# Performance work log

Measured on AMD Instinct MI355X. Metric: run time of the kernel, lower is better.

Reference implementation:

```python
import jax, jax.numpy as jnp
import numpy as np

N = 100000
E = 1600000
ROUND = 2


def spmm(src, dst, x):
    # adj.matmul(x) with binary sparse adjacency given as edge list:
    # out[dst] += x[src]
    return jax.ops.segment_sum(x[src], dst, num_segments=N)


def setup_inputs() -> dict:
    key = jax.random.key(0)
    ks = jax.random.split(key, 8)
    x = jax.random.normal(ks[0], (N, 512), dtype=jnp.float32)
    W_embed = jax.random.normal(ks[1], (512, 64), dtype=jnp.float32) * (1.0 / np.sqrt(512))
    b_embed = jnp.zeros((64,), dtype=jnp.float32)
    W_cls = jax.random.normal(ks[2], (448, 40), dtype=jnp.float32) * (1.0 / np.sqrt(448))
    b_cls = jnp.zeros((40,), dtype=jnp.float32)
    adj_src = jax.random.randint(ks[3], (E,), 0, N, dtype=jnp.int32)
    adj_dst = jax.random.randint(ks[4], (E,), 0, N, dtype=jnp.int32)
    adj2_src = jax.random.randint(ks[5], (E,), 0, N, dtype=jnp.int32)
    adj2_dst = jax.random.randint(ks[6], (E,), 0, N, dtype=jnp.int32)
    return {"x": x, "W_embed": W_embed, "b_embed": b_embed, "W_cls": W_cls,
            "b_cls": b_cls, "adj_src": adj_src, "adj_dst": adj_dst,
            "adj2_src": adj2_src, "adj2_dst": adj2_dst}


def reference(x, W_embed, b_embed, W_cls, b_cls, adj_src, adj_dst, adj2_src, adj2_dst):
    # embed: Linear + ReLU
    h = jax.nn.relu(x @ W_embed + b_embed)  # [N, 64]
    hidden_reps = [h]
    for _ in range(ROUND):
        r1 = spmm(adj_src, adj_dst, h)      # 1-hop aggregation
        r2 = spmm(adj2_src, adj2_dst, h)    # 2-hop aggregation
        h = jnp.concatenate([r1, r2], axis=-1)
        hidden_reps.append(h)
    hf = jnp.concatenate(hidden_reps, axis=-1)  # [N, 64*(2^(ROUND+1)-1)] = [N, 448]
    # dropout is identity in eval mode
    logits = hf @ W_cls + b_cls
    return jax.nn.log_softmax(logits, axis=1)
```

## Files before the change

kernel.cpp:

```cpp
#include <hip/hip_runtime.h>
#include <hip/hip_bf16.h>

#define NN 100000
#define EE 1600000
#define NBK 196
#define BSH 9
#define EPB 4096
#define STG 10240
#define CAP 9216

using frag8 = __attribute__((ext_vector_type(8))) short;
using f32x4 = __attribute__((ext_vector_type(4))) float;

__device__ inline unsigned short f2bf(float f) {
    unsigned u = __float_as_uint(f);
    u = u + 0x7FFFu + ((u >> 16) & 1u);
    return (unsigned short)(u >> 16);
}
__device__ inline float bf2f(unsigned short u) {
    return __uint_as_float(((unsigned)u) << 16);
}
__device__ inline unsigned pack_bf16(float a, float b) {
    __hip_bfloat162 h = __float22bfloat162_rn(float2{a, b});
    union { __hip_bfloat162 h2; unsigned u; } c;
    c.h2 = h;
    return c.u;
}
__device__ inline unsigned char f2fp8(float v) {
    unsigned p = __builtin_amdgcn_cvt_pk_fp8_f32(v, v, 0, false);
    return (unsigned char)(p & 0xff);
}


__global__ __launch_bounds__(256) void binA_k(const int* __restrict__ s1,
                                              const int* __restrict__ d1,
                                              const int* __restrict__ s2,
                                              const int* __restrict__ d2,
                                              int* __restrict__ bcur,
                                              unsigned* __restrict__ tmp1,
                                              unsigned* __restrict__ tmp2) {
    __shared__ int lhist[NBK], lbase[NBK], gbase[NBK], lcur[NBK];
    __shared__ int sscan[256];
    __shared__ int stot;
    __shared__ uint2 stage[EPB];
    int adj = blockIdx.y;
    const int* ss = adj ? s2 : s1;
    const int* dd = adj ? d2 : d1;
    unsigned* tmp = adj ? tmp2 : tmp1;
    int t = threadIdx.x;
    for (int i = t; i < NBK; i += 256) { lhist[i] = 0; lcur[i] = 0; }
    __syncthreads();
    int e0 = blockIdx.x * EPB;
    int d[16], s[16];
    #pragma unroll
    for (int k = 0; k < 16; ++k) {
        int e = e0 + k * 256 + t;
        d[k] = (e < EE) ? dd[e] : -1;
        s[k] = (e < EE) ? ss[e] : 0;
        if (d[k] >= 0) atomicAdd(&lhist[d[k] >> BSH], 1);
    }
    __syncthreads();
    int hv = (t < NBK) ? lhist[t] : 0;
    sscan[t] = hv;
    __syncthreads();
    for (int off = 1; off < 256; off <<= 1) {
        int u = (t >= off) ? sscan[t - off] : 0;
        __syncthreads();
        sscan[t] += u;
        __syncthreads();
    }
    if (t < NBK) lbase[t] = sscan[t] - hv;
    if (t == NBK - 1) stot = sscan[t];
    __syncthreads();
    for (int i = t; i < NBK; i += 256)
        gbase[i] = lhist[i] ? atomicAdd(&bcur[adj * NBK + i], lhist[i]) : 0;
    __syncthreads();
    #pragma unroll
    for (int k = 0; k < 16; ++k) {
        if (d[k] >= 0) {
            int b = d[k] >> BSH;
            int pos = lbase[b] + atomicAdd(&lcur[b], 1);
            stage[pos] = make_uint2((unsigned)d[k], (unsigned)s[k]);
        }
    }
    __syncthreads();
    int tot = stot;
    for (int i = t; i < tot; i += 256) {
        uint2 u = stage[i];
        int b = u.x >> BSH;
        int off = gbase[b] + (i - lbase[b]);
        if (off < CAP)
            tmp[(size_t)b * CAP + off] = ((u.x & 511u) << 17) | u.y;
    }
}

__global__ __launch_bounds__(256) void binB_k(const unsigned* __restrict__ tmp1,
                                              const unsigned* __restrict__ tmp2,
                                              const int* __restrict__ bcur,
                                              int2* __restrict__ rse1,
                                              int2* __restrict__ rse2,
                                              int* __restrict__ csr1,
                                              int* __restrict__ csr2) {
    __shared__ int cnt[512], cur[512];
    __shared__ int sscan[256];
    __shared__ int stage[STG];
    int adj = blockIdx.y, b = blockIdx.x;
    const unsigned* tmp = adj ? tmp2 : tmp1;
    int2* rse = adj ? rse2 : rse1;
    int* csr  = adj ? csr2 : csr1;
    int t = threadIdx.x;
    int n0 = b << BSH;
    int n1 = n0 + 512; if (n1 > NN) n1 = NN;
    int nn = n1 - n0;
    int base = b * CAP;
    int count = bcur[adj * NBK + b];
    if (count > CAP) count = CAP;
    cnt[t] = 0; cnt[t + 256] = 0;
    __syncthreads();
    for (int i = t; i < count; i += 256)
        atomicAdd(&cnt[tmp[base + i] >> 17], 1);
    __syncthreads();
    int c0 = cnt[2 * t], c1 = cnt[2 * t + 1];
    int ps = c0 + c1;
    sscan[t] = ps;
    __syncthreads();
    for (int off = 1; off < 256; off <<= 1) {
        int u = (t >= off) ? sscan[t - off] : 0;
        __syncthreads();
        sscan[t] += u;
        __syncthreads();
    }
    int pe = sscan[t] - ps;
    int e0x = pe, e1x = pe + c0;
    if (2 * t < nn)     rse[n0 + 2 * t]     = make_int2(base + e0x, c0);
    if (2 * t + 1 < nn) rse[n0 + 2 * t + 1] = make_int2(base + e1x, c1);
    cur[2 * t] = e0x; cur[2 * t + 1] = e1x;
    __syncthreads();
    for (int i = t; i < count; i += 256) {
        unsigned u = tmp[base + i];
        int loc = atomicAdd(&cur[u >> 17], 1);
        int src = (int)(u & 0x1FFFFu);
        if (loc < STG) stage[loc] = src;
        else csr[base + loc] = src;
    }
    __syncthreads();
    int m = count < STG ? count : STG;
    for (int i = t; i < m; i += 256) csr[base + i] = stage[i];
}


__global__ void wprep_k(const float* __restrict__ W, unsigned short* __restrict__ Wbf,
                        const float* __restrict__ Wc, unsigned short* __restrict__ Wbig) {
    int blk = blockIdx.x;
    if (blk < 128) {
        int id = blk * 256 + threadIdx.x;
        if (id < 512 * 64) {
            int k = id >> 6, col = id & 63;
            int ch = k >> 3, el = k & 7;
            int cs = (ch & ~15) | ((ch & 15) ^ (col & 7));
            Wbf[col * 512 + cs * 8 + el] = f2bf(W[id]);
        }
    } else {
        int id = (blk - 128) * 256 + threadIdx.x;
        int k = id >> 7, col = id & 127;
        float v = 0.f;
        if (col < 40) v = Wc[k * 40 + col];
        else if (col < 80)  { if (k >= 64) v = Wc[(192 + k - 64) * 40 + (col - 40)]; }
        else if (col < 120) { if (k >= 64) v = Wc[(320 + k - 64) * 40 + (col - 80)]; }
        int ch = k >> 3, el = k & 7;
        int phys = (ch & ~7) | ((ch & 7) ^ (col & 7));
        Wbig[col * 192 + phys * 8 + el] = f2bf(v);
    }
}


__global__ __launch_bounds__(256) void embed_k(const float* __restrict__ x,
                                               const unsigned short* __restrict__ Wbf,
                                               const float* __restrict__ bias,
                                               unsigned short* __restrict__ hcat,
                                               unsigned char* __restrict__ h0f8) {
    __shared__ unsigned short sW[64 * 128];
    int tid = threadIdx.x;
    int lane = tid & 63, wave = tid >> 6;
    int row0 = blockIdx.x * 64;
    f32x4 acc[4];
    #pragma unroll
    for (int n = 0; n < 4; n++) acc[n] = (f32x4){0.f, 0.f, 0.f, 0.f};

    int arow = row0 + wave * 16 + (lane & 15);
    bool valid = arow < NN;
    const float* xrow = x + (size_t)(valid ? arow : 0) * 512 + (lane >> 4) * 8;

    for (int kt = 0; kt < 4; ++kt) {
        for (int q = tid; q < 1024; q += 256) {
            int col = q >> 4, c = q & 15;
            ((uint4*)sW)[q] = ((const uint4*)Wbf)[col * 64 + kt * 16 + c];
        }
        __syncthreads();
        #pragma unroll
        for (int kk = 0; kk < 4; ++kk) {
            const float4* px = (const float4*)(xrow + kt * 128 + kk * 32);
            float4 p0 = px[0], p1 = px[1];
            frag8 a;
            unsigned* au = (unsigned*)&a;
            if (valid) {
                au[0] = pack_bf16(p0.x, p0.y);
                au[1] = pack_bf16(p0.z, p0.w);
                au[2] = pack_bf16(p1.x, p1.y);
                au[3] = pack_bf16(p1.z, p1.w);
            } else {
                au[0] = 0; au[1] = 0; au[2] = 0; au[3] = 0;
            }
            #pragma unroll
            for (int n = 0; n < 4; n++) {
                int col = n * 16 + (lane & 15);
                int bc = (kk * 4 + (lane >> 4)) ^ (col & 7);
                frag8 b = *(const frag8*)&sW[(col * 16 + bc) * 8];
                acc[n] = __builtin_amdgcn_mfma_f32_16x16x32_bf16(a, b, acc[n], 0, 0, 0);
            }
        }
        __syncthreads();
    }
    #pragma unroll
    for (int n = 0; n < 4; n++) {
        int col = n * 16 + (lane & 15);
        float bv = bias[col];
        #pragma unroll
        for (int i = 0; i < 4; i++) {
            int r = row0 + wave * 16 + (lane >> 4) * 4 + i;
            if (r < NN) {
                float vv = acc[n][i] + bv;
                vv = vv > 0.f ? vv : 0.f;
                hcat[(size_t)r * 192 + col] = f2bf(vv);
                h0f8[(size_t)r * 64 + col] = f2fp8(vv);
            }
        }
    }
}


__device__ inline void gacc8f8(float* a, uint2 u) {
    a[0] += __builtin_amdgcn_cvt_f32_fp8(u.x, 0);
    a[1] += __builtin_amdgcn_cvt_f32_fp8(u.x, 1);
    a[2] += __builtin_amdgcn_cvt_f32_fp8(u.x, 2);
    a[3] += __builtin_amdgcn_cvt_f32_fp8(u.x, 3);
    a[4] += __builtin_amdgcn_cvt_f32_fp8(u.y, 0);
    a[5] += __builtin_amdgcn_cvt_f32_fp8(u.y, 1);
    a[6] += __builtin_amdgcn_cvt_f32_fp8(u.y, 2);
    a[7] += __builtin_amdgcn_cvt_f32_fp8(u.y, 3);
}


__global__ __launch_bounds__(256) void round1_k(const unsigned char* __restrict__ h8,
                                                unsigned short* __restrict__ hc,
                                                const int2* __restrict__ rse1,
                                                const int* __restrict__ csr1,
                                                const int2* __restrict__ rse2,
                                                const int* __restrict__ csr2) {
    int wave = threadIdx.x >> 6, lane = threadIdx.x & 63;
    int row = blockIdx.x * 4 + wave;
    int g = lane >> 3, gl = lane & 7;

    int2 v1r = rse1[row], v2r = rse2[row];
    int s1 = v1r.x, c1 = v1r.y, e1 = s1 + c1;
    int s2 = v2r.x, c2 = v2r.y, e2 = s2 + c2;
    int idx1 = 0, idx2 = 0;
    if (lane < c1) idx1 = csr1[s1 + lane];
    if (lane < c2) idx2 = csr2[s2 + lane];
    int cnt1 = c1 < 64 ? c1 : 64, cnt2 = c2 < 64 ? c2 : 64;

    float a1[8] = {0.f, 0.f, 0.f, 0.f, 0.f, 0.f, 0.f, 0.f};
    float a2[8] = {0.f, 0.f, 0.f, 0.f, 0.f, 0.f, 0.f, 0.f};

    {
        int j0 = g, j1 = 8 + g;
        int x10 = __shfl(idx1, j0), x11 = __shfl(idx1, j1);
        int x20 = __shfl(idx2, j0), x21 = __shfl(idx2, j1);
        uint2 u10 = *((const uint2*)(h8 + (size_t)x10 * 64) + gl);
        uint2 u11 = *((const uint2*)(h8 + (size_t)x11 * 64) + gl);
        uint2 u20 = *((const uint2*)(h8 + (size_t)x20 * 64) + gl);
        uint2 u21 = *((const uint2*)(h8 + (size_t)x21 * 64) + gl);
        if (j0 < cnt1) gacc8f8(a1, u10);
        if (j1 < cnt1) gacc8f8(a1, u11);
        if (j0 < cnt2) gacc8f8(a2, u20);
        if (j1 < cnt2) gacc8f8(a2, u21);
    }
    int nq1 = (cnt1 + 7) >> 3, nq2 = (cnt2 + 7) >> 3;
    int nq = nq1 > nq2 ? nq1 : nq2;
    for (int q = 2; q < nq; ++q) {
        int j = q * 8 + g;
        int y1 = __shfl(idx1, j), y2 = __shfl(idx2, j);
        uint2 w1 = *((const uint2*)(h8 + (size_t)y1 * 64) + gl);
        uint2 w2 = *((const uint2*)(h8 + (size_t)y2 * 64) + gl);
        if (j < cnt1) gacc8f8(a1, w1);
        if (j < cnt2) gacc8f8(a2, w2);
    }
    for (int t0 = s1 + 64; t0 < e1; t0 += 64) {
        int rem = e1 - t0;
        int idxv = 0;
        if (lane < rem) idxv = csr1[t0 + lane];
        int cnt = rem < 64 ? rem : 64;
        int nqt = (cnt + 7) >> 3;
        for (int q = 0; q < nqt; ++q) {
            int j = q * 8 + g;
            int s0 = __shfl(idxv, j);
            uint2 u = *((const uint2*)(h8 + (size_t)s0 * 64) + gl);
            if (j < cnt) gacc8f8(a1, u);
        }
    }
    for (int t0 = s2 + 64; t0 < e2; t0 += 64) {
        int rem = e2 - t0;
        int idxv = 0;
        if (lane < rem) idxv = csr2[t0 + lane];
        int cnt = rem < 64 ? rem : 64;
        int nqt = (cnt + 7) >> 3;
        for (int q = 0; q < nqt; ++q) {
            int j = q * 8 + g;
            int s0 = __shfl(idxv, j);
            uint2 u = *((const uint2*)(h8 + (size_t)s0 * 64) + gl);
            if (j < cnt) gacc8f8(a2, u);
        }
    }

    #pragma unroll
    for (int i = 0; i < 8; ++i) {
        a1[i] += __shfl_xor(a1[i], 8);
        a1[i] += __shfl_xor(a1[i], 16);
        a1[i] += __shfl_xor(a1[i], 32);
        a2[i] += __shfl_xor(a2[i], 8);
        a2[i] += __shfl_xor(a2[i], 16);
        a2[i] += __shfl_xor(a2[i], 32);
    }
    if (lane < 8) {
        uint4 o;
        o.x = pack_bf16(a1[0], a1[1]);
        o.y = pack_bf16(a1[2], a1[3]);
        o.z = pack_bf16(a1[4], a1[5]);
        o.w = pack_bf16(a1[6], a1[7]);
        *(uint4*)(hc + (size_t)row * 192 + 64 + lane * 8) = o;
    } else if (lane < 16) {
        int l = lane - 8;
        uint4 o;
        o.x = pack_bf16(a2[0], a2[1]);
        o.y = pack_bf16(a2[2], a2[3]);
        o.z = pack_bf16(a2[4], a2[5]);
        o.w = pack_bf16(a2[6], a2[7]);
        *(uint4*)(hc + (size_t)row * 192 + 128 + l * 8) = o;
    }
}


__global__ __launch_bounds__(256) void gemm_k(const unsigned short* __restrict__ hcat,
                                              const unsigned short* __restrict__ Wbig,
                                              const float* __restrict__ bc,
                                              float* __restrict__ logits,
                                              unsigned char* __restrict__ zf8) {
    __shared__ unsigned short sA[64 * 64];
    __shared__ unsigned short sB[128 * 64];
    int tid = threadIdx.x;
    int lane = tid & 63, wave = tid >> 6;
    int row0 = blockIdx.x * 64;
    f32x4 acc[8];
    #pragma unroll
    for (int n = 0; n < 8; n++) acc[n] = (f32x4){0.f, 0.f, 0.f, 0.f};

    for (int kt = 0; kt < 3; ++kt) {
        #pragma unroll
        for (int q = tid; q < 512; q += 256) {
            int r = q >> 3, c = q & 7;
            int phys = c ^ (r & 7);
            ((uint4*)sA)[r * 8 + phys] = ((const uint4*)hcat)[(size_t)(row0 + r) * 24 + kt * 8 + c];
        }
        #pragma unroll
        for (int q = tid; q < 1024; q += 256) {
            int col = q >> 3, c = q & 7;
            ((uint4*)sB)[q] = ((const uint4*)Wbig)[col * 24 + kt * 8 + c];
        }
        __syncthreads();
        #pragma unroll
        for (int kk = 0; kk < 2; ++kk) {
            int ar = wave * 16 + (lane & 15);
            int ac = (kk * 4 + (lane >> 4)) ^ (ar & 7);
            frag8 a = *(const frag8*)&sA[(ar * 8 + ac) * 8];
            #pragma unroll
            for (int n = 0; n < 8; n++) {
                int col = n * 16 + (lane & 15);
                int bcc = (kk * 4 + (lane >> 4)) ^ (col & 7);
                frag8 b = *(const frag8*)&sB[(col * 8 + bcc) * 8];
                acc[n] = __builtin_amdgcn_mfma_f32_16x16x32_bf16(a, b, acc[n], 0, 0, 0);
            }
        }
        __syncthreads();
    }
    #pragma unroll
    for (int n = 0; n < 8; n++) {
        int col = n * 16 + (lane & 15);
        float bv = (col < 40) ? bc[col] : 0.f;
        #pragma unroll
        for (int i = 0; i < 4; i++) {
            int r = row0 + wave * 16 + (lane >> 4) * 4 + i;
            if (r < NN) {
                float vv = acc[n][i];
                if (col < 40) {
                    logits[(size_t)r * 40 + col] = vv + bv;
                } else if (col < 80) {
                    zf8[(size_t)r * 128 + (col - 40)] = f2fp8(vv);
                } else if (col < 120) {
                    zf8[(size_t)r * 128 + 64 + (col - 80)] = f2fp8(vv);
                }
            }
        }
    }
}


__global__ __launch_bounds__(256) void round2_k(const unsigned char* __restrict__ z8,
                                                const int2* __restrict__ rse1,
                                                const int* __restrict__ csr1,
                                                const int2* __restrict__ rse2,
                                                const int* __restrict__ csr2,
                                                float* __restrict__ logits) {
    int wave = threadIdx.x >> 6, lane = threadIdx.x & 63;
    int row = blockIdx.x * 4 + wave;
    int g = lane >> 3, gl = lane & 7;

    int2 v1r = rse1[row], v2r = rse2[row];
    int s1 = v1r.x, c1 = v1r.y, e1 = s1 + c1;
    int s2 = v2r.x, c2 = v2r.y, e2 = s2 + c2;
    int idx1 = 0, idx2 = 0;
    if (lane < c1) idx1 = csr1[s1 + lane];
    if (lane < c2) idx2 = csr2[s2 + lane];
    int cnt1 = c1 < 64 ? c1 : 64, cnt2 = c2 < 64 ? c2 : 64;

    float a[8] = {0.f, 0.f, 0.f, 0.f, 0.f, 0.f, 0.f, 0.f};

    {
        int j0 = g, j1 = 8 + g;
        int x10 = __shfl(idx1, j0), x11 = __shfl(idx1, j1);
        int x20 = __shfl(idx2, j0), x21 = __shfl(idx2, j1);
        uint2 u10 = *((const uint2*)(z8 + (size_t)x10 * 128) + gl);
        uint2 u11 = *((const uint2*)(z8 + (size_t)x11 * 128) + gl);
        uint2 u20 = *((const uint2*)(z8 + (size_t)x20 * 128 + 64) + gl);
        uint2 u21 = *((const uint2*)(z8 + (size_t)x21 * 128 + 64) + gl);
        if (j0 < cnt1) gacc8f8(a, u10);
        if (j1 < cnt1) gacc8f8(a, u11);
        if (j0 < cnt2) gacc8f8(a, u20);
        if (j1 < cnt2) gacc8f8(a, u21);
    }
    int nq1 = (cnt1 + 7) >> 3, nq2 = (cnt2 + 7) >> 3;
    int nq = nq1 > nq2 ? nq1 : nq2;
    for (int q = 2; q < nq; ++q) {
        int j = q * 8 + g;
        int y1 = __shfl(idx1, j), y2 = __shfl(idx2, j);
        uint2 w1 = *((const uint2*)(z8 + (size_t)y1 * 128) + gl);
        uint2 w2 = *((const uint2*)(z8 + (size_t)y2 * 128 + 64) + gl);
        if (j < cnt1) gacc8f8(a, w1);
        if (j < cnt2) gacc8f8(a, w2);
    }
    for (int t0 = s1 + 64; t0 < e1; t0 += 64) {
        int rem = e1 - t0;
        int idxv = 0;
        if (lane < rem) idxv = csr1[t0 + lane];
        int cnt = rem < 64 ? rem : 64;
        int nqt = (cnt + 7) >> 3;
        for (int q = 0; q < nqt; ++q) {
            int j = q * 8 + g;
            int s0 = __shfl(idxv, j);
            uint2 u = *((const uint2*)(z8 + (size_t)s0 * 128) + gl);
            if (j < cnt) gacc8f8(a, u);
        }
    }
    for (int t0 = s2 + 64; t0 < e2; t0 += 64) {
        int rem = e2 - t0;
        int idxv = 0;
        if (lane < rem) idxv = csr2[t0 + lane];
        int cnt = rem < 64 ? rem : 64;
        int nqt = (cnt + 7) >> 3;
        for (int q = 0; q < nqt; ++q) {
            int j = q * 8 + g;
            int s0 = __shfl(idxv, j);
            uint2 u = *((const uint2*)(z8 + (size_t)s0 * 128 + 64) + gl);
            if (j < cnt) gacc8f8(a, u);
        }
    }

    #pragma unroll
    for (int i = 0; i < 8; ++i) {
        a[i] += __shfl_xor(a[i], 8);
        a[i] += __shfl_xor(a[i], 16);
        a[i] += __shfl_xor(a[i], 32);
    }

    bool act = lane < 5;
    float v[8];
    if (act) {
        float4 b0 = *(const float4*)(logits + (size_t)row * 40 + lane * 8);
        float4 b1 = *(const float4*)(logits + (size_t)row * 40 + lane * 8 + 4);
        v[0] = b0.x + a[0]; v[1] = b0.y + a[1]; v[2] = b0.z + a[2]; v[3] = b0.w + a[3];
        v[4] = b1.x + a[4]; v[5] = b1.y + a[5]; v[6] = b1.z + a[6]; v[7] = b1.w + a[7];
    } else {
        #pragma unroll
        for (int i = 0; i < 8; ++i) v[i] = -1e30f;
    }
    float m = fmaxf(fmaxf(fmaxf(v[0], v[1]), fmaxf(v[2], v[3])),
                    fmaxf(fmaxf(v[4], v[5]), fmaxf(v[6], v[7])));
    m = fmaxf(m, __shfl_xor(m, 1));
    m = fmaxf(m, __shfl_xor(m, 2));
    m = fmaxf(m, __shfl_xor(m, 4));
    float es = 0.f;
    if (act) {
        #pragma unroll
        for (int i = 0; i < 8; ++i) es += __expf(v[i] - m);
    }
    es += __shfl_xor(es, 1);
    es += __shfl_xor(es, 2);
    es += __shfl_xor(es, 4);
    float ls = __logf(es);
    if (act) {
        float4 o0, o1;
        o0.x = v[0] - m - ls; o0.y = v[1] - m - ls; o0.z = v[2] - m - ls; o0.w = v[3] - m - ls;
        o1.x = v[4] - m - ls; o1.y = v[5] - m - ls; o1.z = v[6] - m - ls; o1.w = v[7] - m - ls;
        *(float4*)(logits + (size_t)row * 40 + lane * 8)     = o0;
        *(float4*)(logits + (size_t)row * 40 + lane * 8 + 4) = o1;
    }
}


extern "C" void kernel_launch(void* const* d_in, const int* in_sizes, int n_in,
                              void* d_out, int out_size, void* d_ws, size_t ws_size,
                              hipStream_t stream) {
    const float* x       = (const float*)d_in[0];
    const float* W_embed = (const float*)d_in[1];
    const float* b_embed = (const float*)d_in[2];
    const float* W_cls   = (const float*)d_in[3];
    const float* b_cls   = (const float*)d_in[4];
    const int* a1src = (const int*)d_in[5];
    const int* a1dst = (const int*)d_in[6];
    const int* a2src = (const int*)d_in[7];
    const int* a2dst = (const int*)d_in[8];

    float* logits = (float*)d_out;
    float* ws = (float*)d_ws;

    const size_t OFF_HCAT = 0;
    const size_t OFF_H0F8 = 9600000;
    const size_t OFF_ZF8  = 11200000;
    const size_t OFF_RSE1 = 14400000;
    const size_t OFF_RSE2 = 14600000;
    const size_t OFF_BC   = 14800000;
    const size_t OFF_CSR1 = 14800392;
    const size_t OFF_CSR2 = 16606728;
    const size_t OFF_TMP1 = 18413064;
    const size_t OFF_TMP2 = 20219400;
    const size_t OFF_WBF  = 22025736;
    const size_t OFF_WBIG = 22042120;

    unsigned short* hcat = (unsigned short*)(ws + OFF_HCAT);
    unsigned char*  h0f8 = (unsigned char*)(ws + OFF_H0F8);
    unsigned char*  zf8  = (unsigned char*)(ws + OFF_ZF8);
    int2* rse1 = (int2*)(ws + OFF_RSE1);
    int2* rse2 = (int2*)(ws + OFF_RSE2);
    int*  bcur = (int*)(ws + OFF_BC);
    int*  csr1 = (int*)(ws + OFF_CSR1);
    int*  csr2 = (int*)(ws + OFF_CSR2);
    unsigned* tmp1 = (unsigned*)(ws + OFF_TMP1);
    unsigned* tmp2 = (unsigned*)(ws + OFF_TMP2);
    unsigned short* wbf  = (unsigned short*)(ws + OFF_WBF);
    unsigned short* wbig = (unsigned short*)(ws + OFF_WBIG);

    hipMemsetAsync(ws + OFF_BC, 0, 392 * 4, stream);

    const int NBA = (EE + EPB - 1) / EPB;

    binA_k<<<dim3(NBA, 2), 256, 0, stream>>>(a1src, a1dst, a2src, a2dst, bcur, tmp1, tmp2);
    binB_k<<<dim3(NBK, 2), 256, 0, stream>>>(tmp1, tmp2, bcur, rse1, rse2, csr1, csr2);

    wprep_k<<<224, 256, 0, stream>>>(W_embed, wbf, W_cls, wbig);
    embed_k<<<(NN + 63) / 64, 256, 0, stream>>>(x, wbf, b_embed, hcat, h0f8);

    round1_k<<<NN / 4, 256, 0, stream>>>(h0f8, hcat, rse1, csr1, rse2, csr2);
    gemm_k<<<(NN + 63) / 64, 256, 0, stream>>>(hcat, wbig, b_cls, logits, zf8);
    round2_k<<<NN / 4, 256, 0, stream>>>(zf8, rse1, csr1, rse2, csr2, logits);
}
```

Baseline: 252.9 us.

## Merge prep kernels horizontally and widen gather loads to 16-byte per lane

Merges the edge-binning and weight-prep kernels into one launch, and the CSR build and embedding GEMM into a second launch, so independent work shares a grid and two launches go away. The CSR build drops its shared-memory staging and writes straight to global memory. The gather kernels now have each lane load 16 fp8 bytes instead of 8, so 16 neighbours are processed per wave step instead of 8. The wider loads mean fewer load instructions and fewer loop iterations, but one more shuffle-reduction stage and more registers per lane.

Result: slower. 379.9 us (+50.2%).

```diff
diff --git a/kernel.cpp b/kernel.cpp
--- a/kernel.cpp
+++ b/kernel.cpp
@@ -6,7 +6,7 @@
 #define NBK 196
 #define BSH 9
 #define EPB 4096
-#define STG 10240
+#define NBA 391
 #define CAP 9216
 
 using frag8 = __attribute__((ext_vector_type(8))) short;
@@ -16,9 +16,6 @@
     unsigned u = __float_as_uint(f);
     u = u + 0x7FFFu + ((u >> 16) & 1u);
     return (unsigned short)(u >> 16);
-}
-__device__ inline float bf2f(unsigned short u) {
-    return __uint_as_float(((unsigned)u) << 16);
 }
 __device__ inline unsigned pack_bf16(float a, float b) {
     __hip_bfloat162 h = __float22bfloat162_rn(float2{a, b});
@@ -32,25 +29,56 @@
 }
 
 
-__global__ __launch_bounds__(256) void binA_k(const int* __restrict__ s1,
-                                              const int* __restrict__ d1,
-                                              const int* __restrict__ s2,
-                                              const int* __restrict__ d2,
-                                              int* __restrict__ bcur,
-                                              unsigned* __restrict__ tmp1,
-                                              unsigned* __restrict__ tmp2) {
+__global__ __launch_bounds__(256) void prep1_k(const int* __restrict__ s1,
+                                               const int* __restrict__ d1,
+                                               const int* __restrict__ s2,
+                                               const int* __restrict__ d2,
+                                               int* __restrict__ bcur,
+                                               unsigned* __restrict__ tmp1,
+                                               unsigned* __restrict__ tmp2,
+                                               const float* __restrict__ W,
+                                               unsigned short* __restrict__ Wbf,
+                                               const float* __restrict__ Wc,
+                                               unsigned short* __restrict__ Wbig) {
     __shared__ int lhist[NBK], lbase[NBK], gbase[NBK], lcur[NBK];
     __shared__ int sscan[256];
     __shared__ int stot;
     __shared__ uint2 stage[EPB];
-    int adj = blockIdx.y;
+    int blk = blockIdx.x;
+    int t = threadIdx.x;
+
+    if (blk >= 2 * NBA) {
+        int wb = blk - 2 * NBA;
+        if (wb < 128) {
+            int id = wb * 256 + t;
+            if (id < 512 * 64) {
+                int k = id >> 6, col = id & 63;
+                int ch = k >> 3, el = k & 7;
+                int cs = (ch & ~15) | ((ch & 15) ^ (col & 7));
+                Wbf[col * 512 + cs * 8 + el] = f2bf(W[id]);
+            }
+        } else {
+            int id = (wb - 128) * 256 + t;
+            int k = id >> 7, col = id & 127;
+            float v = 0.f;
+            if (col < 40) v = Wc[k * 40 + col];
+            else if (col < 80)  { if (k >= 64) v = Wc[(192 + k - 64) * 40 + (col - 40)]; }
+            else if (col < 120) { if (k >= 64) v = Wc[(320 + k - 64) * 40 + (col - 80)]; }
+            int ch = k >> 3, el = k & 7;
+            int phys = (ch & ~7) | ((ch & 7) ^ (col & 7));
+            Wbig[col * 192 + phys * 8 + el] = f2bf(v);
+        }
+        return;
+    }
+
+    int adj = blk / NBA;
+    int chunk = blk % NBA;
     const int* ss = adj ? s2 : s1;
     const int* dd = adj ? d2 : d1;
     unsigned* tmp = adj ? tmp2 : tmp1;
-    int t = threadIdx.x;
     for (int i = t; i < NBK; i += 256) { lhist[i] = 0; lcur[i] = 0; }
     __syncthreads();
-    int e0 = blockIdx.x * EPB;
+    int e0 = chunk * EPB;
     int d[16], s[16];
     #pragma unroll
     for (int k = 0; k < 16; ++k) {
@@ -94,95 +122,67 @@
     }
 }
 
-__global__ __launch_bounds__(256) void binB_k(const unsigned* __restrict__ tmp1,
-                                              const unsigned* __restrict__ tmp2,
-                                              const int* __restrict__ bcur,
-                                              int2* __restrict__ rse1,
-                                              int2* __restrict__ rse2,
-                                              int* __restrict__ csr1,
-                                              int* __restrict__ csr2) {
-    __shared__ int cnt[512], cur[512];
-    __shared__ int sscan[256];
-    __shared__ int stage[STG];
-    int adj = blockIdx.y, b = blockIdx.x;
-    const unsigned* tmp = adj ? tmp2 : tmp1;
-    int2* rse = adj ? rse2 : rse1;
-    int* csr  = adj ? csr2 : csr1;
-    int t = threadIdx.x;
-    int n0 = b << BSH;
-    int n1 = n0 + 512; if (n1 > NN) n1 = NN;
-    int nn = n1 - n0;
-    int base = b * CAP;
-    int count = bcur[adj * NBK + b];
-    if (count > CAP) count = CAP;
-    cnt[t] = 0; cnt[t + 256] = 0;
-    __syncthreads();
-    for (int i = t; i < count; i += 256)
-        atomicAdd(&cnt[tmp[base + i] >> 17], 1);
-    __syncthreads();
-    int c0 = cnt[2 * t], c1 = cnt[2 * t + 1];
-    int ps = c0 + c1;
-    sscan[t] = ps;
-    __syncthreads();
-    for (int off = 1; off < 256; off <<= 1) {
-        int u = (t >= off) ? sscan[t - off] : 0;
-        __syncthreads();
-        sscan[t] += u;
-        __syncthreads();
-    }
-    int pe = sscan[t] - ps;
-    int e0x = pe, e1x = pe + c0;
-    if (2 * t < nn)     rse[n0 + 2 * t]     = make_int2(base + e0x, c0);
-    if (2 * t + 1 < nn) rse[n0 + 2 * t + 1] = make_int2(base + e1x, c1);
-    cur[2 * t] = e0x; cur[2 * t + 1] = e1x;
-    __syncthreads();
-    for (int i = t; i < count; i += 256) {
-        unsigned u = tmp[base + i];
-        int loc = atomicAdd(&cur[u >> 17], 1);
-        int src = (int)(u & 0x1FFFFu);
-        if (loc < STG) stage[loc] = src;
-        else csr[base + loc] = src;
-    }
-    __syncthreads();
-    int m = count < STG ? count : STG;
-    for (int i = t; i < m; i += 256) csr[base + i] = stage[i];
-}
-
-
-__global__ void wprep_k(const float* __restrict__ W, unsigned short* __restrict__ Wbf,
-                        const float* __restrict__ Wc, unsigned short* __restrict__ Wbig) {
-    int blk = blockIdx.x;
-    if (blk < 128) {
-        int id = blk * 256 + threadIdx.x;
-        if (id < 512 * 64) {
-            int k = id >> 6, col = id & 63;
-            int ch = k >> 3, el = k & 7;
-            int cs = (ch & ~15) | ((ch & 15) ^ (col & 7));
-            Wbf[col * 512 + cs * 8 + el] = f2bf(W[id]);
-        }
-    } else {
-        int id = (blk - 128) * 256 + threadIdx.x;
-        int k = id >> 7, col = id & 127;
-        float v = 0.f;
-        if (col < 40) v = Wc[k * 40 + col];
-        else if (col < 80)  { if (k >= 64) v = Wc[(192 + k - 64) * 40 + (col - 40)]; }
-        else if (col < 120) { if (k >= 64) v = Wc[(320 + k - 64) * 40 + (col - 80)]; }
-        int ch = k >> 3, el = k & 7;
-        int phys = (ch & ~7) | ((ch & 7) ^ (col & 7));
-        Wbig[col * 192 + phys * 8 + el] = f2bf(v);
-    }
-}
-
-
-__global__ __launch_bounds__(256) void embed_k(const float* __restrict__ x,
+
+__global__ __launch_bounds__(256) void prep2_k(const unsigned* __restrict__ tmp1,
+                                               const unsigned* __restrict__ tmp2,
+                                               const int* __restrict__ bcur,
+                                               int2* __restrict__ rse1,
+                                               int2* __restrict__ rse2,
+                                               int* __restrict__ csr1,
+                                               int* __restrict__ csr2,
+                                               const float* __restrict__ x,
                                                const unsigned short* __restrict__ Wbf,
                                                const float* __restrict__ bias,
                                                unsigned short* __restrict__ hcat,
                                                unsigned char* __restrict__ h0f8) {
+    __shared__ int cnt[512], cur[512];
+    __shared__ int sscan[256];
     __shared__ unsigned short sW[64 * 128];
-    int tid = threadIdx.x;
-    int lane = tid & 63, wave = tid >> 6;
-    int row0 = blockIdx.x * 64;
+    int blk = blockIdx.x;
+    int t = threadIdx.x;
+
+    if (blk < 2 * NBK) {
+        int adj = blk / NBK, b = blk % NBK;
+        const unsigned* tmp = adj ? tmp2 : tmp1;
+        int2* rse = adj ? rse2 : rse1;
+        int* csr  = adj ? csr2 : csr1;
+        int n0 = b << BSH;
+        int n1 = n0 + 512; if (n1 > NN) n1 = NN;
+        int nn = n1 - n0;
+        int base = b * CAP;
+        int count = bcur[adj * NBK + b];
+        if (count > CAP) count = CAP;
+        cnt[t] = 0; cnt[t + 256] = 0;
+        __syncthreads();
+        for (int i = t; i < count; i += 256)
+            atomicAdd(&cnt[tmp[base + i] >> 17], 1);
+        __syncthreads();
+        int c0 = cnt[2 * t], c1 = cnt[2 * t + 1];
+        int ps = c0 + c1;
+        sscan[t] = ps;
+        __syncthreads();
+        for (int off = 1; off < 256; off <<= 1) {
+            int u = (t >= off) ? sscan[t - off] : 0;
+            __syncthreads();
+            sscan[t] += u;
+            __syncthreads();
+        }
+        int pe = sscan[t] - ps;
+        int e0x = pe, e1x = pe + c0;
+        if (2 * t < nn)     rse[n0 + 2 * t]     = make_int2(base + e0x, c0);
+        if (2 * t + 1 < nn) rse[n0 + 2 * t + 1] = make_int2(base + e1x, c1);
+        cur[2 * t] = e0x; cur[2 * t + 1] = e1x;
+        __syncthreads();
+        for (int i = t; i < count; i += 256) {
+            unsigned u = tmp[base + i];
+            int loc = atomicAdd(&cur[u >> 17], 1);
+            csr[base + loc] = (int)(u & 0x1FFFFu);
+        }
+        return;
+    }
+
+    int lane = t & 63, wave = t >> 6;
+    int row0 = (blk - 2 * NBK) * 64;
     f32x4 acc[4];
     #pragma unroll
     for (int n = 0; n < 4; n++) acc[n] = (f32x4){0.f, 0.f, 0.f, 0.f};
@@ -192,7 +192,7 @@
     const float* xrow = x + (size_t)(valid ? arow : 0) * 512 + (lane >> 4) * 8;
 
     for (int kt = 0; kt < 4; ++kt) {
-        for (int q = tid; q < 1024; q += 256) {
+        for (int q = t; q < 1024; q += 256) {
             int col = q >> 4, c = q & 15;
             ((uint4*)sW)[q] = ((const uint4*)Wbf)[col * 64 + kt * 16 + c];
         }
@@ -215,8 +215,8 @@
             for (int n = 0; n < 4; n++) {
                 int col = n * 16 + (lane & 15);
                 int bc = (kk * 4 + (lane >> 4)) ^ (col & 7);
-                frag8 b = *(const frag8*)&sW[(col * 16 + bc) * 8];
-                acc[n] = __builtin_amdgcn_mfma_f32_16x16x32_bf16(a, b, acc[n], 0, 0, 0);
+                frag8 bfr = *(const frag8*)&sW[(col * 16 + bc) * 8];
+                acc[n] = __builtin_amdgcn_mfma_f32_16x16x32_bf16(a, bfr, acc[n], 0, 0, 0);
             }
         }
         __syncthreads();
@@ -239,15 +239,23 @@
 }
 
 
-__device__ inline void gacc8f8(float* a, uint2 u) {
-    a[0] += __builtin_amdgcn_cvt_f32_fp8(u.x, 0);
-    a[1] += __builtin_amdgcn_cvt_f32_fp8(u.x, 1);
-    a[2] += __builtin_amdgcn_cvt_f32_fp8(u.x, 2);
-    a[3] += __builtin_amdgcn_cvt_f32_fp8(u.x, 3);
-    a[4] += __builtin_amdgcn_cvt_f32_fp8(u.y, 0);
-    a[5] += __builtin_amdgcn_cvt_f32_fp8(u.y, 1);
-    a[6] += __builtin_amdgcn_cvt_f32_fp8(u.y, 2);
-    a[7] += __builtin_amdgcn_cvt_f32_fp8(u.y, 3);
+__device__ inline void gacc16f8(float* a, uint4 u) {
+    a[0]  += __builtin_amdgcn_cvt_f32_fp8(u.x, 0);
+    a[1]  += __builtin_amdgcn_cvt_f32_fp8(u.x, 1);
+    a[2]  += __builtin_amdgcn_cvt_f32_fp8(u.x, 2);
+    a[3]  += __builtin_amdgcn_cvt_f32_fp8(u.x, 3);
+    a[4]  += __builtin_amdgcn_cvt_f32_fp8(u.y, 0);
+    a[5]  += __builtin_amdgcn_cvt_f32_fp8(u.y, 1);
+    a[6]  += __builtin_amdgcn_cvt_f32_fp8(u.y, 2);
+    a[7]  += __builtin_amdgcn_cvt_f32_fp8(u.y, 3);
+    a[8]  += __builtin_amdgcn_cvt_f32_fp8(u.z, 0);
+    a[9]  += __builtin_amdgcn_cvt_f32_fp8(u.z, 1);
+    a[10] += __builtin_amdgcn_cvt_f32_fp8(u.z, 2);
+    a[11] += __builtin_amdgcn_cvt_f32_fp8(u.z, 3);
+    a[12] += __builtin_amdgcn_cvt_f32_fp8(u.w, 0);
+    a[13] += __builtin_amdgcn_cvt_f32_fp8(u.w, 1);
+    a[14] += __builtin_amdgcn_cvt_f32_fp8(u.w, 2);
+    a[15] += __builtin_amdgcn_cvt_f32_fp8(u.w, 3);
 }
 
 
@@ -259,7 +267,7 @@
                                                 const int* __restrict__ csr2) {
     int wave = threadIdx.x >> 6, lane = threadIdx.x & 63;
     int row = blockIdx.x * 4 + wave;
-    int g = lane >> 3, gl = lane & 7;
+    int slot = lane >> 2, sub = lane & 3;
 
     int2 v1r = rse1[row], v2r = rse2[row];
     int s1 = v1r.x, c1 = v1r.y, e1 = s1 + c1;
@@ -269,43 +277,39 @@
     if (lane < c2) idx2 = csr2[s2 + lane];
     int cnt1 = c1 < 64 ? c1 : 64, cnt2 = c2 < 64 ? c2 : 64;
 
-    float a1[8] = {0.f, 0.f, 0.f, 0.f, 0.f, 0.f, 0.f, 0.f};
-    float a2[8] = {0.f, 0.f, 0.f, 0.f, 0.f, 0.f, 0.f, 0.f};
+    float a1[16], a2[16];
+    #pragma unroll
+    for (int i = 0; i < 16; ++i) { a1[i] = 0.f; a2[i] = 0.f; }
 
     {
-        int j0 = g, j1 = 8 + g;
-        int x10 = __shfl(idx1, j0), x11 = __shfl(idx1, j1);
-        int x20 = __shfl(idx2, j0), x21 = __shfl(idx2, j1);
-        uint2 u10 = *((const uint2*)(h8 + (size_t)x10 * 64) + gl);
-        uint2 u11 = *((const uint2*)(h8 + (size_t)x11 * 64) + gl);
-        uint2 u20 = *((const uint2*)(h8 + (size_t)x20 * 64) + gl);
-        uint2 u21 = *((const uint2*)(h8 + (size_t)x21 * 64) + gl);
-        if (j0 < cnt1) gacc8f8(a1, u10);
-        if (j1 < cnt1) gacc8f8(a1, u11);
-        if (j0 < cnt2) gacc8f8(a2, u20);
-        if (j1 < cnt2) gacc8f8(a2, u21);
-    }
-    int nq1 = (cnt1 + 7) >> 3, nq2 = (cnt2 + 7) >> 3;
+        int x1 = __shfl(idx1, slot);
+        int x2 = __shfl(idx2, slot);
+        uint4 u1 = *((const uint4*)(h8 + (size_t)x1 * 64) + sub);
+        uint4 u2 = *((const uint4*)(h8 + (size_t)x2 * 64) + sub);
+        if (slot < cnt1) gacc16f8(a1, u1);
+        if (slot < cnt2) gacc16f8(a2, u2);
+    }
+    int nq1 = (cnt1 + 15) >> 4, nq2 = (cnt2 + 15) >> 4;
     int nq = nq1 > nq2 ? nq1 : nq2;
-    for (int q = 2; q < nq; ++q) {
-        int j = q * 8 + g;
+    for (int q = 1; q < nq; ++q) {
+        int j = q * 16 + slot;
         int y1 = __shfl(idx1, j), y2 = __shfl(idx2, j);
-        uint2 w1 = *((const uint2*)(h8 + (size_t)y1 * 64) + gl);
-        uint2 w2 = *((const uint2*)(h8 + (size_t)y2 * 64) + gl);
-        if (j < cnt1) gacc8f8(a1, w1);
-        if (j < cnt2) gacc8f8(a2, w2);
+        uint4 w1 = *((const uint4*)(h8 + (size_t)y1 * 64) + sub);
+        uint4 w2 = *((const uint4*)(h8 + (size_t)y2 * 64) + sub);
+        if (j < cnt1) gacc16f8(a1, w1);
+        if (j < cnt2) gacc16f8(a2, w2);
     }
     for (int t0 = s1 + 64; t0 < e1; t0 += 64) {
         int rem = e1 - t0;
         int idxv = 0;
         if (lane < rem) idxv = csr1[t0 + lane];
         int cnt = rem < 64 ? rem : 64;
-        int nqt = (cnt + 7) >> 3;
+        int nqt = (cnt + 15) >> 4;
         for (int q = 0; q < nqt; ++q) {
-            int j = q * 8 + g;
+            int j = q * 16 + slot;
             int s0 = __shfl(idxv, j);
-            uint2 u = *((const uint2*)(h8 + (size_t)s0 * 64) + gl);
-            if (j < cnt) gacc8f8(a1, u);
+            uint4 u = *((const uint4*)(h8 + (size_t)s0 * 64) + sub);
+            if (j < cnt) gacc16f8(a1, u);
         }
     }
     for (int t0 = s2 + 64; t0 < e2; t0 += 64) {
@@ -313,39 +317,36 @@
         int idxv = 0;
         if (lane < rem) idxv = csr2[t0 + lane];
         int cnt = rem < 64 ? rem : 64;
-        int nqt = (cnt + 7) >> 3;
+        int nqt = (cnt + 15) >> 4;
         for (int q = 0; q < nqt; ++q) {
-            int j = q * 8 + g;
+            int j = q * 16 + slot;
             int s0 = __shfl(idxv, j);
-            uint2 u = *((const uint2*)(h8 + (size_t)s0 * 64) + gl);
-            if (j < cnt) gacc8f8(a2, u);
-        }
-    }
-
-    #pragma unroll
-    for (int i = 0; i < 8; ++i) {
-        a1[i] += __shfl_xor(a1[i], 8);
-        a1[i] += __shfl_xor(a1[i], 16);
-        a1[i] += __shfl_xor(a1[i], 32);
-        a2[i] += __shfl_xor(a2[i], 8);
-        a2[i] += __shfl_xor(a2[i], 16);
-        a2[i] += __shfl_xor(a2[i], 32);
-    }
-    if (lane < 8) {
-        uint4 o;
-        o.x = pack_bf16(a1[0], a1[1]);
-        o.y = pack_bf16(a1[2], a1[3]);
-        o.z = pack_bf16(a1[4], a1[5]);
-        o.w = pack_bf16(a1[6], a1[7]);
-        *(uint4*)(hc + (size_t)row * 192 + 64 + lane * 8) = o;
-    } else if (lane < 16) {
-        int l = lane - 8;
-        uint4 o;
-        o.x = pack_bf16(a2[0], a2[1]);
-        o.y = pack_bf16(a2[2], a2[3]);
-        o.z = pack_bf16(a2[4], a2[5]);
-        o.w = pack_bf16(a2[6], a2[7]);
-        *(uint4*)(hc + (size_t)row * 192 + 128 + l * 8) = o;
+            uint4 u = *((const uint4*)(h8 + (size_t)s0 * 64) + sub);
+            if (j < cnt) gacc16f8(a2, u);
+        }
+    }
+
+    #pragma unroll
+    for (int i = 0; i < 16; ++i) {
+        a1[i] += __shfl_xor(a1[i], 4);  a1[i] += __shfl_xor(a1[i], 8);
+        a1[i] += __shfl_xor(a1[i], 16); a1[i] += __shfl_xor(a1[i], 32);
+        a2[i] += __shfl_xor(a2[i], 4);  a2[i] += __shfl_xor(a2[i], 8);
+        a2[i] += __shfl_xor(a2[i], 16); a2[i] += __shfl_xor(a2[i], 32);
+    }
+    if (slot == 0) {
+        uint4 lo, hi;
+        lo.x = pack_bf16(a1[0],  a1[1]);  lo.y = pack_bf16(a1[2],  a1[3]);
+        lo.z = pack_bf16(a1[4],  a1[5]);  lo.w = pack_bf16(a1[6],  a1[7]);
+        hi.x = pack_bf16(a1[8],  a1[9]);  hi.y = pack_bf16(a1[10], a1[11]);
+        hi.z = pack_bf16(a1[12], a1[13]); hi.w = pack_bf16(a1[14], a1[15]);
+        *(uint4*)(hc + (size_t)row * 192 + 64 + sub * 16)     = lo;
+        *(uint4*)(hc + (size_t)row * 192 + 64 + sub * 16 + 8) = hi;
+        lo.x = pack_bf16(a2[0],  a2[1]);  lo.y = pack_bf16(a2[2],  a2[3]);
+        lo.z = pack_bf16(a2[4],  a2[5]);  lo.w = pack_bf16(a2[6],  a2[7]);
+        hi.x = pack_bf16(a2[8],  a2[9]);  hi.y = pack_bf16(a2[10], a2[11]);
+        hi.z = pack_bf16(a2[12], a2[13]); hi.w = pack_bf16(a2[14], a2[15]);
+        *(uint4*)(hc + (size_t)row * 192 + 128 + sub * 16)     = lo;
+        *(uint4*)(hc + (size_t)row * 192 + 128 + sub * 16 + 8) = hi;
     }
 }
 
@@ -422,7 +423,7 @@
                                                 float* __restrict__ logits) {
     int wave = threadIdx.x >> 6, lane = threadIdx.x & 63;
     int row = blockIdx.x * 4 + wave;
-    int g = lane >> 3, gl = lane & 7;
+    int slot = lane >> 2, sub = lane & 3;
 
     int2 v1r = rse1[row], v2r = rse2[row];
     int s1 = v1r.x, c1 = v1r.y, e1 = s1 + c1;
@@ -432,42 +433,39 @@
     if (lane < c2) idx2 = csr2[s2 + lane];
     int cnt1 = c1 < 64 ? c1 : 64, cnt2 = c2 < 64 ? c2 : 64;
 
-    float a[8] = {0.f, 0.f, 0.f, 0.f, 0.f, 0.f, 0.f, 0.f};
+    float a[16];
+    #pragma unroll
+    for (int i = 0; i < 16; ++i) a[i] = 0.f;
 
     {
-        int j0 = g, j1 = 8 + g;
-        int x10 = __shfl(idx1, j0), x11 = __shfl(idx1, j1);
-        int x20 = __shfl(idx2, j0), x21 = __shfl(idx2, j1);
-        uint2 u10 = *((const uint2*)(z8 + (size_t)x10 * 128) + gl);
-        uint2 u11 = *((const uint2*)(z8 + (size_t)x11 * 128) + gl);
-        uint2 u20 = *((const uint2*)(z8 + (size_t)x20 * 128 + 64) + gl);
-        uint2 u21 = *((const uint2*)(z8 + (size_t)x21 * 128 + 64) + gl);
-        if (j0 < cnt1) gacc8f8(a, u10);
-        if (j1 < cnt1) gacc8f8(a, u11);
-        if (j0 < cnt2) gacc8f8(a, u20);
-        if (j1 < cnt2) gacc8f8(a, u21);
-    }
-    int nq1 = (cnt1 + 7) >> 3, nq2 = (cnt2 + 7) >> 3;
+        int x1 = __shfl(idx1, slot);
+        int x2 = __shfl(idx2, slot);
+        uint4 u1 = *((const uint4*)(z8 + (size_t)x1 * 128) + sub);
+        uint4 u2 = *((const uint4*)(z8 + (size_t)x2 * 128 + 64) + sub);
+        if (slot < cnt1) gacc16f8(a, u1);
+        if (slot < cnt2) gacc16f8(a, u2);
+    }
+    int nq1 = (cnt1 + 15) >> 4, nq2 = (cnt2 + 15) >> 4;
     int nq = nq1 > nq2 ? nq1 : nq2;
-    for (int q = 2; q < nq; ++q) {
-        int j = q * 8 + g;
+    for (int q = 1; q < nq; ++q) {
+        int j = q * 16 + slot;
         int y1 = __shfl(idx1, j), y2 = __shfl(idx2, j);
-        uint2 w1 = *((const uint2*)(z8 + (size_t)y1 * 128) + gl);
-        uint2 w2 = *((const uint2*)(z8 + (size_t)y2 * 128 + 64) + gl);
-        if (j < cnt1) gacc8f8(a, w1);
-        if (j < cnt2) gacc8f8(a, w2);
+        uint4 w1 = *((const uint4*)(z8 + (size_t)y1 * 128) + sub);
+        uint4 w2 = *((const uint4*)(z8 + (size_t)y2 * 128 + 64) + sub);
+        if (j < cnt1) gacc16f8(a, w1);
+        if (j < cnt2) gacc16f8(a, w2);
     }
     for (int t0 = s1 + 64; t0 < e1; t0 += 64) {
         int rem = e1 - t0;
         int idxv = 0;
         if (lane < rem) idxv = csr1[t0 + lane];
         int cnt = rem < 64 ? rem : 64;
-        int nqt = (cnt + 7) >> 3;
+        int nqt = (cnt + 15) >> 4;
         for (int q = 0; q < nqt; ++q) {
-            int j = q * 8 + g;
+            int j = q * 16 + slot;
             int s0 = __shfl(idxv, j);
-            uint2 u = *((const uint2*)(z8 + (size_t)s0 * 128) + gl);
-            if (j < cnt) gacc8f8(a, u);
+            uint4 u = *((const uint4*)(z8 + (size_t)s0 * 128) + sub);
+            if (j < cnt) gacc16f8(a, u);
         }
     }
     for (int t0 = s2 + 64; t0 < e2; t0 += 64) {
@@ -475,53 +473,52 @@
         int idxv = 0;
         if (lane < rem) idxv = csr2[t0 + lane];
         int cnt = rem < 64 ? rem : 64;
-        int nqt = (cnt + 7) >> 3;
+        int nqt = (cnt + 15) >> 4;
         for (int q = 0; q < nqt; ++q) {
-            int j = q * 8 + g;
+            int j = q * 16 + slot;
             int s0 = __shfl(idxv, j);
-            uint2 u = *((const uint2*)(z8 + (size_t)s0 * 128 + 64) + gl);
-            if (j < cnt) gacc8f8(a, u);
-        }
-    }
-
-    #pragma unroll
-    for (int i = 0; i < 8; ++i) {
-        a[i] += __shfl_xor(a[i], 8);
-        a[i] += __shfl_xor(a[i], 16);
-        a[i] += __shfl_xor(a[i], 32);
-    }
-
-    bool act = lane < 5;
-    float v[8];
-    if (act) {
-        float4 b0 = *(const float4*)(logits + (size_t)row * 40 + lane * 8);
-        float4 b1 = *(const float4*)(logits + (size_t)row * 40 + lane * 8 + 4);
-        v[0] = b0.x + a[0]; v[1] = b0.y + a[1]; v[2] = b0.z + a[2]; v[3] = b0.w + a[3];
-        v[4] = b1.x + a[4]; v[5] = b1.y + a[5]; v[6] = b1.z + a[6]; v[7] = b1.w + a[7];
-    } else {
-        #pragma unroll
-        for (int i = 0; i < 8; ++i) v[i] = -1e30f;
-    }
-    float m = fmaxf(fmaxf(fmaxf(v[0], v[1]), fmaxf(v[2], v[3])),
-                    fmaxf(fmaxf(v[4], v[5]), fmaxf(v[6], v[7])));
+            uint4 u = *((const uint4*)(z8 + (size_t)s0 * 128 + 64) + sub);
+            if (j < cnt) gacc16f8(a, u);
+        }
+    }
+
+    #pragma unroll
+    for (int i = 0; i < 16; ++i) {
+        a[i] += __shfl_xor(a[i], 4);  a[i] += __shfl_xor(a[i], 8);
+        a[i] += __shfl_xor(a[i], 16); a[i] += __shfl_xor(a[i], 32);
+    }
+
+    int nv = sub == 0 ? 16 : (sub == 1 ? 16 : (sub == 2 ? 8 : 0));
+    bool wr = (slot == 0) && (nv > 0);
+    float v[16];
+    #pragma unroll
+    for (int i = 0; i < 16; ++i) v[i] = -1e30f;
+    if (wr) {
+        for (int i = 0; i < nv; i += 4) {
+            float4 b0 = *(const float4*)(logits + (size_t)row * 40 + sub * 16 + i);
+            v[i] = b0.x + a[i]; v[i + 1] = b0.y + a[i + 1];
+            v[i + 2] = b0.z + a[i + 2]; v[i + 3] = b0.w + a[i + 3];
+        }
+    }
+    float m = v[0];
+    #pragma unroll
+    for (int i = 1; i < 16; ++i) m = fmaxf(m, v[i]);
     m = fmaxf(m, __shfl_xor(m, 1));
     m = fmaxf(m, __shfl_xor(m, 2));
-    m = fmaxf(m, __shfl_xor(m, 4));
     float es = 0.f;
-    if (act) {
-        #pragma unroll
-        for (int i = 0; i < 8; ++i) es += __expf(v[i] - m);
+    if (wr) {
+        for (int i = 0; i < nv; ++i) es += __expf(v[i] - m);
     }
     es += __shfl_xor(es, 1);
     es += __shfl_xor(es, 2);
-    es += __shfl_xor(es, 4);
     float ls = __logf(es);
-    if (act) {
-        float4 o0, o1;
-        o0.x = v[0] - m - ls; o0.y = v[1] - m - ls; o0.z = v[2] - m - ls; o0.w = v[3] - m - ls;
-        o1.x = v[4] - m - ls; o1.y = v[5] - m - ls; o1.z = v[6] - m - ls; o1.w = v[7] - m - ls;
-        *(float4*)(logits + (size_t)row * 40 + lane * 8)     = o0;
-        *(float4*)(logits + (size_t)row * 40 + lane * 8 + 4) = o1;
+    if (wr) {
+        for (int i = 0; i < nv; i += 4) {
+            float4 o;
+            o.x = v[i] - m - ls;     o.y = v[i + 1] - m - ls;
+            o.z = v[i + 2] - m - ls; o.w = v[i + 3] - m - ls;
+            *(float4*)(logits + (size_t)row * 40 + sub * 16 + i) = o;
+        }
     }
 }
 
@@ -570,13 +567,11 @@
 
     hipMemsetAsync(ws + OFF_BC, 0, 392 * 4, stream);
 
-    const int NBA = (EE + EPB - 1) / EPB;
-
-    binA_k<<<dim3(NBA, 2), 256, 0, stream>>>(a1src, a1dst, a2src, a2dst, bcur, tmp1, tmp2);
-    binB_k<<<dim3(NBK, 2), 256, 0, stream>>>(tmp1, tmp2, bcur, rse1, rse2, csr1, csr2);
-
-    wprep_k<<<224, 256, 0, stream>>>(W_embed, wbf, W_cls, wbig);
-    embed_k<<<(NN + 63) / 64, 256, 0, stream>>>(x, wbf, b_embed, hcat, h0f8);
+    prep1_k<<<2 * NBA + 224, 256, 0, stream>>>(a1src, a1dst, a2src, a2dst, bcur, tmp1, tmp2,
+                                               W_embed, wbf, W_cls, wbig);
+    prep2_k<<<2 * NBK + (NN + 63) / 64, 256, 0, stream>>>(tmp1, tmp2, bcur,
+                                                          rse1, rse2, csr1, csr2,
+                                                          x, wbf, b_embed, hcat, h0f8);
 
     round1_k<<<NN / 4, 256, 0, stream>>>(h0f8, hcat, rse1, csr1, rse2, csr2);
     gemm_k<<<(NN + 63) / 64, 256, 0, stream>>>(hcat, wbig, b_cls, logits, zf8);
```
